# Optimization experiments

Measured on AMD Instinct MI355X. Metric: run time of the kernel, lower is better.

## Reference

```python
import jax, jax.numpy as jnp
import numpy as np

B, H, V, L, M, D, C = 64, 512, 50000, 400, 128, 64, 64
HC = 2 * D + M + 4  # controller LSTM hidden size (one head)
EPS = 1e-8


def _lstm_step(x, h, c, Wih, Whh, bih, bhh):
    g = x @ Wih.T + bih + h @ Whh.T + bhh
    i, f, gg, o = jnp.split(g, 4, axis=-1)
    c2 = jax.nn.sigmoid(f) * c + jax.nn.sigmoid(i) * jnp.tanh(gg)
    return jax.nn.sigmoid(o) * jnp.tanh(c2), c2


def _head_params(hc):
    # slices exactly as in LSTMMemoryController (k=0, single head)
    keys = hc[:, :M]                               # [B, M]
    kstr = jnp.exp(hc[:, D:D + 1])                 # [B, 1]
    gate = jax.nn.sigmoid(hc[:, D + 1:D + 2])      # [B, 1]
    erase = jax.nn.sigmoid(hc[:, D + 4:M + D + 4]) # [B, M]
    add = jax.nn.sigmoid(hc[:, 2 * D + 4:M + 2 * D + 4])  # [B, M]
    return keys, kstr, gate, erase, add


def _addressing(keys, kstr, gate, heads, memory):
    # torch cosine_similarity(keys.unsqueeze(2), memory, dim=2):
    # keys [B,M] broadcast along memory_dim D
    num = keys * memory.sum(-1)                                   # [B, M]
    nk = jnp.maximum(jnp.abs(keys) * jnp.sqrt(jnp.float32(D)), EPS)
    nm = jnp.maximum(jnp.linalg.norm(memory, axis=-1), EPS)
    cos = num / (nk * nm)
    content = jax.nn.softmax(kstr * cos, axis=1)                  # [B, M]
    # faithful to original: heads[k] indexes axis 0 (k=0) -> shape [1, M]
    gated = gate * content + (1.0 - gate) * heads[0]
    return gated[:, None, :]                                      # [B, 1, M]


def reference(input_ids, h0, c0, encoder_outputs, word_occurrence_indicator,
              coverage, memory, read_heads, write_heads,
              read_h, read_c, write_h, write_c,
              emb, attn_W, attn_b, cov_W, state_W, comb_W, comb_b,
              rpre_W, rpre_b, wpre_W, wpre_b,
              r_Wih, r_Whh, r_bih, r_bhh,
              w_Wih, w_Whh, w_bih, w_bhh,
              l_Wih, l_Whh, l_bih, l_bhh,
              out_W, out_b):
    embedded = emb[input_ids]                                     # [B, H]
    ia = jnp.concatenate([embedded, h0], 1) @ attn_W.T + attn_b  # [B, L]
    tc = (coverage + ia) @ cov_W.T
    ts = c0 @ state_W.T
    aw = jax.nn.softmax(tc + ia + ts, axis=1)                     # [B, L]
    attn_applied = jnp.einsum('bl,blh->bh', aw, encoder_outputs)  # [B, H]
    out0 = jnp.concatenate([embedded, attn_applied], 1) @ comb_W.T + comb_b  # [B, H]

    hm = jnp.concatenate([h0, memory.reshape(-1, M * D)], 1)
    rh, rc = _lstm_step(hm @ rpre_W.T + rpre_b, read_h, read_c, r_Wih, r_Whh, r_bih, r_bhh)
    wh, wc = _lstm_step(hm @ wpre_W.T + wpre_b, write_h, write_c, w_Wih, w_Whh, w_bih, w_bhh)
    rk, rks, rg, _, _ = _head_params(rh)
    wk, wks, wg, we, wa = _head_params(wh)
    rw = _addressing(rk, rks, rg, read_heads, memory)             # [B, 1, M]
    ww = _addressing(wk, wks, wg, write_heads, memory)            # [B, 1, M]

    read_in = jnp.einsum('bkm,bmd->bkd', rw, memory).reshape(-1, D)
    h1, c1 = _lstm_step(jnp.concatenate([out0, read_in], 1), h0, c0,
                        l_Wih, l_Whh, l_bih, l_bhh)
    # residual (h1 + out0) is computed in the original but unused by its output path

    w0 = ww[:, 0, :, None]                                        # [B, M, 1]
    new_memory = memory * (1.0 - w0 * we[:, :, None]) + w0 * wa[:, :, None]
    new_coverage = coverage + ia

    log_probs = jax.nn.log_softmax(c1[:, None, :] @ out_W.T + out_b, axis=-1)  # [B, 1, V]
    return log_probs, h1, c1, new_memory, new_coverage


def setup_inputs() -> dict:
    key = jax.random.key(0)
    ks = iter(jax.random.split(key, 48))

    def rn(shape, fan_in):
        return jax.random.normal(next(ks), shape, jnp.float32) / np.sqrt(fan_in)

    inp = {
        'input_ids': jax.random.randint(next(ks), (B,), 0, V),
        'h0': jax.random.normal(next(ks), (B, H), jnp.float32),
        'c0': jax.random.normal(next(ks), (B, H), jnp.float32),
        'encoder_outputs': jax.random.normal(next(ks), (B, L, H), jnp.float32),
        'word_occurrence_indicator': jnp.zeros((B, L), jnp.float32),
        'coverage': jnp.zeros((B, L), jnp.float32),
        'memory': jax.random.normal(next(ks), (B, M, D), jnp.float32),
        'read_heads': jnp.zeros((B, 1, M), jnp.float32),
        'write_heads': jnp.zeros((B, 1, M), jnp.float32),
        'read_h': jnp.zeros((B, HC), jnp.float32),
        'read_c': jnp.zeros((B, HC), jnp.float32),
        'write_h': jnp.zeros((B, HC), jnp.float32),
        'write_c': jnp.zeros((B, HC), jnp.float32),
        'emb': rn((V, H), H),
        'attn_W': rn((L, 2 * H), 2 * H), 'attn_b': jnp.zeros((L,), jnp.float32),
        'cov_W': rn((L, L), L),
        'state_W': rn((L, H), H),
        'comb_W': rn((H, 2 * H), 2 * H), 'comb_b': jnp.zeros((H,), jnp.float32),
        'rpre_W': rn((C, M * D + H), M * D + H), 'rpre_b': jnp.zeros((C,), jnp.float32),
        'wpre_W': rn((C, M * D + H), M * D + H), 'wpre_b': jnp.zeros((C,), jnp.float32),
        'r_Wih': rn((4 * HC, C), C), 'r_Whh': rn((4 * HC, HC), HC),
        'r_bih': jnp.zeros((4 * HC,), jnp.float32), 'r_bhh': jnp.zeros((4 * HC,), jnp.float32),
        'w_Wih': rn((4 * HC, C), C), 'w_Whh': rn((4 * HC, HC), HC),
        'w_bih': jnp.zeros((4 * HC,), jnp.float32), 'w_bhh': jnp.zeros((4 * HC,), jnp.float32),
        'l_Wih': rn((4 * H, H + D), H + D), 'l_Whh': rn((4 * H, H), H),
        'l_bih': jnp.zeros((4 * H,), jnp.float32), 'l_bhh': jnp.zeros((4 * H,), jnp.float32),
        'out_W': rn((V, H), H), 'out_b': jnp.zeros((V,), jnp.float32),
    }
    return inp
```

## Files before the change

### kernel.cpp

```cpp
#include <hip/hip_runtime.h>
#include <math.h>

#define BB 64
#define HH 512
#define VV 50000
#define LL 400
#define MM 128
#define DD 64
#define HC 260
#define EPSF 1e-8f

typedef __attribute__((ext_vector_type(8))) short bf16x8;
typedef __attribute__((ext_vector_type(4))) float f32x4;
typedef __attribute__((address_space(1))) const void CGV;
typedef __attribute__((address_space(3))) void LV;

__device__ __forceinline__ float sigmoidf(float x){ return 1.0f/(1.0f+expf(-x)); }
__device__ __forceinline__ unsigned short bf16_rne(float f){
  unsigned u = __float_as_uint(f);
  return (unsigned short)((u + 0x7fffu + ((u >> 16) & 1u)) >> 16);
}
__device__ __forceinline__ float wave_max(float v){
  #pragma unroll
  for(int o=32;o;o>>=1) v = fmaxf(v, __shfl_xor(v,o));
  return v;
}
__device__ __forceinline__ float wave_sum(float v){
  #pragma unroll
  for(int o=32;o;o>>=1) v += __shfl_xor(v,o);
  return v;
}

__global__ void k_embed(const int* __restrict__ ids, const float* __restrict__ emb,
                        const float* __restrict__ h0, float* __restrict__ xcat1,
                        float* __restrict__ xcat2){
  int idx = blockIdx.x*256 + threadIdx.x;
  if (idx >= BB*HH) return;
  int b = idx >> 9, h = idx & 511;
  float e = emb[(long)ids[b]*HH + h];
  xcat1[b*1024 + h] = e;
  xcat2[b*1024 + h] = e;
  xcat1[b*1024 + 512 + h] = h0[idx];
}

template<int NB, int FUSE>
__global__ __launch_bounds__(256) void k_gemv(const float* __restrict__ A,
                                              const float* __restrict__ A2,
                                              const float* __restrict__ W,
                                              const float* __restrict__ b1,
                                              float* __restrict__ C,
                                              int K, int N, int ldc){
  int b = blockIdx.y;
  int wid = threadIdx.x >> 6, lane = threadIdx.x & 63;
  int n = blockIdx.x*4 + wid;
  if (n >= N) return;
  const float4* A4  = (const float4*)(A + (long)b*K);
  const float4* A24 = (const float4*)(A2 + (long)b*K);
  const float4* W4  = (const float4*)(W + (long)n*K);
  int K4 = K >> 2;
  float acc = 0.f;
  for (int k = lane; k < K4; k += 64){
    float4 a = A4[k];
    if (FUSE){ float4 a2 = A24[k]; a.x+=a2.x; a.y+=a2.y; a.z+=a2.z; a.w+=a2.w; }
    float4 w = W4[k];
    acc += a.x*w.x + a.y*w.y + a.z*w.z + a.w*w.w;
  }
  acc = wave_sum(acc);
  if (lane == 0){
    if (NB) acc += b1[n];
    C[(long)b*ldc + n] = acc;
  }
}

__global__ void k_cov(const float* __restrict__ cov, const float* __restrict__ ia,
                      float* __restrict__ out){
  int idx = blockIdx.x*256 + threadIdx.x;
  if (idx >= BB*LL) return;
  out[idx] = cov[idx] + ia[idx];
}

__global__ __launch_bounds__(256) void k_softmax_aw(const float* __restrict__ ia,
                                                    const float* __restrict__ ts,
                                                    const float* __restrict__ tc,
                                                    float* __restrict__ aw){
  int b = blockIdx.x, t = threadIdx.x;
  int i0 = t, i1 = t + 256;
  float x0 = ia[b*LL+i0] + ts[b*LL+i0] + tc[b*LL+i0];
  float x1 = (i1 < LL) ? (ia[b*LL+i1] + ts[b*LL+i1] + tc[b*LL+i1]) : -INFINITY;
  __shared__ float sm[4], ss[4];
  float m = wave_max(fmaxf(x0, x1));
  if ((t & 63) == 0) sm[t>>6] = m;
  __syncthreads();
  m = fmaxf(fmaxf(sm[0], sm[1]), fmaxf(sm[2], sm[3]));
  float e0 = expf(x0 - m);
  float e1 = (i1 < LL) ? expf(x1 - m) : 0.0f;
  float s = wave_sum(e0 + e1);
  if ((t & 63) == 0) ss[t>>6] = s;
  __syncthreads();
  float tot = ss[0] + ss[1] + ss[2] + ss[3];
  float inv = 1.0f / tot;
  aw[b*LL + i0] = e0 * inv;
  if (i1 < LL) aw[b*LL + i1] = e1 * inv;
}

__global__ __launch_bounds__(256) void k_attn_part(const float* __restrict__ aw,
                                                   const float* __restrict__ enc,
                                                   float* __restrict__ part){
  int b = blockIdx.x, lc = blockIdx.y, t = threadIdx.x;
  const float* awb = aw + b*LL + lc*25;
  const float* eb  = enc + ((long)b*LL + lc*25)*HH;
  float a0 = 0.f, a1 = 0.f;
  for (int l = 0; l < 25; l++){
    float a = awb[l];
    a0 += a * eb[(long)l*HH + t];
    a1 += a * eb[(long)l*HH + t + 256];
  }
  part[((b*16 + lc) << 9) + t]       = a0;
  part[((b*16 + lc) << 9) + t + 256] = a1;
}

__global__ void k_attn_reduce(const float* __restrict__ part, float* __restrict__ xcat2){
  int idx = blockIdx.x*256 + threadIdx.x;
  if (idx >= BB*HH) return;
  int b = idx >> 9, h = idx & 511;
  float s = 0.f;
  #pragma unroll
  for (int lc = 0; lc < 16; lc++) s += part[((b*16 + lc) << 9) + h];
  xcat2[b*1024 + 512 + h] = s;
}

__global__ __launch_bounds__(256) void k_pre_gemv(const float* __restrict__ h0,
                                                  const float* __restrict__ mem,
                                                  const float* __restrict__ rW,
                                                  const float* __restrict__ wW,
                                                  float* __restrict__ part){
  int wid = threadIdx.x >> 6, lane = threadIdx.x & 63;
  int n = blockIdx.x*4 + wid;
  int b = blockIdx.y;
  int z = blockIdx.z;
  int which = z >> 3, chunk = z & 7;
  const float* W = which ? wW : rW;
  const float4* W4 = (const float4*)(W + (long)n*8704 + chunk*1088);
  const float4* H4 = (const float4*)(h0 + (long)b*HH);
  const float4* M4 = (const float4*)(mem + (long)b*8192 + (chunk*1088 - 512));
  float acc = 0.f;
  #pragma unroll
  for (int i = 0; i < 5; i++){
    int k4 = lane + i*64;
    if (k4 < 272){
      int kg4 = chunk*272 + k4;
      float4 a = (kg4 < 128) ? H4[kg4] : M4[k4];
      float4 w = W4[k4];
      acc += a.x*w.x + a.y*w.y + a.z*w.z + a.w*w.w;
    }
  }
  acc = wave_sum(acc);
  if (lane == 0) part[z*4096 + b*64 + n] = acc;
}

__global__ void k_pre_reduce(const float* __restrict__ part, const float* __restrict__ rb,
                             const float* __restrict__ wb, float* __restrict__ pre_r,
                             float* __restrict__ pre_w){
  int idx = blockIdx.x*256 + threadIdx.x;
  if (idx >= 8192) return;
  int which = idx >> 12;
  int r = idx & 4095;
  float s = 0.f;
  #pragma unroll
  for (int c = 0; c < 8; c++) s += part[((which<<3)+c)*4096 + r];
  int n = r & 63;
  s += which ? wb[n] : rb[n];
  (which ? pre_w : pre_r)[r] = s;
}

__global__ __launch_bounds__(256) void k_gates_rw(const float* __restrict__ pre_r,
    const float* __restrict__ pre_w, const float* __restrict__ read_h,
    const float* __restrict__ write_h,
    const float* __restrict__ rWih, const float* __restrict__ rWhh,
    const float* __restrict__ rbih, const float* __restrict__ rbhh,
    const float* __restrict__ wWih, const float* __restrict__ wWhh,
    const float* __restrict__ wbih, const float* __restrict__ wbhh,
    float* __restrict__ g_r, float* __restrict__ g_w){
  int which = blockIdx.z;
  int b = blockIdx.y;
  int wid = threadIdx.x >> 6, lane = threadIdx.x & 63;
  int n = blockIdx.x*4 + wid;
  const float* pre = which ? pre_w : pre_r;
  const float* hh  = which ? write_h : read_h;
  const float* Wih = which ? wWih : rWih;
  const float* Whh = which ? wWhh : rWhh;
  float acc = pre[b*64 + lane] * Wih[n*64 + lane];
  const float* hb = hh + b*HC;
  const float* wr = Whh + (long)n*HC;
  #pragma unroll
  for (int i = 0; i < 5; i++){
    int k = lane + i*64;
    if (k < HC) acc += hb[k]*wr[k];
  }
  acc = wave_sum(acc);
  if (lane == 0){
    acc += (which ? wbih : rbih)[n] + (which ? wbhh : rbhh)[n];
    (which ? g_w : g_r)[(long)b*4*HC + n] = acc;
  }
}

__global__ void k_lstm_rw(const float* __restrict__ g_r, const float* __restrict__ g_w,
                          const float* __restrict__ read_c, const float* __restrict__ write_c,
                          float* __restrict__ rh, float* __restrict__ wh){
  int idx = blockIdx.x*256 + threadIdx.x;
  if (idx >= 2*BB*HC) return;
  int which = idx >= BB*HC;
  int r = which ? idx - BB*HC : idx;
  int b = r / HC, j = r - b*HC;
  const float* g = (which ? g_w : g_r) + (long)b*4*HC;
  float c2 = sigmoidf(g[HC + j]) * (which ? write_c : read_c)[r]
           + sigmoidf(g[j]) * tanhf(g[2*HC + j]);
  (which ? wh : rh)[r] = sigmoidf(g[3*HC + j]) * tanhf(c2);
}

__global__ __launch_bounds__(128) void k_address(const float* __restrict__ rh,
                                                 const float* __restrict__ whv,
                                                 const float* __restrict__ rheads,
                                                 const float* __restrict__ wheads,
                                                 const float* __restrict__ mem,
                                                 float* __restrict__ rwout,
                                                 float* __restrict__ wwout){
  int which = blockIdx.y;
  int b = blockIdx.x, m = threadIdx.x;
  const float* hc = which ? whv : rh;
  const float* heads0 = which ? wheads : rheads;
  float* wout = which ? wwout : rwout;
  const float* mr = mem + ((long)b*MM + m)*DD;
  float s = 0.f, q = 0.f;
  #pragma unroll 8
  for (int d = 0; d < DD; d++){ float v = mr[d]; s += v; q += v*v; }
  float key  = hc[b*HC + m];
  float kstr = expf(hc[b*HC + 64]);
  float gate = sigmoidf(hc[b*HC + 65]);
  float nk = fmaxf(fabsf(key)*8.0f, EPSF);
  float nm = fmaxf(sqrtf(q), EPSF);
  float z  = kstr * (key*s) / (nk*nm);
  __shared__ float sm[2], ss[2];
  float mx = wave_max(z);
  if ((m & 63) == 0) sm[m>>6] = mx;
  __syncthreads();
  mx = fmaxf(sm[0], sm[1]);
  float e = expf(z - mx);
  float w = wave_sum(e);
  if ((m & 63) == 0) ss[m>>6] = w;
  __syncthreads();
  float content = e / (ss[0] + ss[1]);
  wout[b*MM + m] = gate*content + (1.0f - gate)*heads0[m];
}

__global__ void k_readin(const float* __restrict__ rw, const float* __restrict__ mem,
                         float* __restrict__ xcat3){
  int b = blockIdx.x, d = threadIdx.x;
  float s = 0.f;
  for (int m = 0; m < MM; m++) s += rw[b*MM + m] * mem[((long)b*MM + m)*DD + d];
  xcat3[b*576 + 512 + d] = s;
}

__global__ void k_newmem(const float* __restrict__ mem, const float* __restrict__ ww,
                         const float* __restrict__ wh, float* __restrict__ out){
  int idx = blockIdx.x*256 + threadIdx.x;
  if (idx >= BB*MM*DD) return;
  int b = idx >> 13;
  int m = (idx & 8191) >> 6;
  float w0 = ww[b*MM + m];
  float we = sigmoidf(wh[b*HC + 68 + m]);
  float wa = sigmoidf(wh[b*HC + 132 + m]);
  out[idx] = mem[idx]*(1.0f - w0*we) + w0*wa;
}

__global__ __launch_bounds__(256) void k_lstm_main(const float* __restrict__ xcat3,
                                                   const float* __restrict__ h0,
                                                   const float* __restrict__ lWih,
                                                   const float* __restrict__ lWhh,
                                                   const float* __restrict__ bih,
                                                   const float* __restrict__ bhh,
                                                   const float* __restrict__ c0,
                                                   float* __restrict__ h1,
                                                   float* __restrict__ c1,
                                                   unsigned short* __restrict__ c1b){
  int wid = threadIdx.x >> 6, lane = threadIdx.x & 63;
  int j = blockIdx.x*4 + wid;
  int b = blockIdx.y;
  const float4* A1 = (const float4*)(xcat3 + (long)b*576);
  const float4* A2 = (const float4*)(h0 + (long)b*HH);
  float gv[4];
  #pragma unroll
  for (int g = 0; g < 4; g++){
    int n = g*HH + j;
    const float4* W1 = (const float4*)(lWih + (long)n*576);
    const float4* W2 = (const float4*)(lWhh + (long)n*HH);
    float s = 0.f;
    #pragma unroll
    for (int i = 0; i < 3; i++){
      int k = lane + i*64;
      if (k < 144){ float4 a = A1[k], w = W1[k]; s += a.x*w.x + a.y*w.y + a.z*w.z + a.w*w.w; }
    }
    #pragma unroll
    for (int i = 0; i < 2; i++){
      int k = lane + i*64;
      float4 a = A2[k], w = W2[k]; s += a.x*w.x + a.y*w.y + a.z*w.z + a.w*w.w;
    }
    gv[g] = wave_sum(s);
  }
  if (lane == 0){
    #pragma unroll
    for (int g = 0; g < 4; g++){ int n = g*HH + j; gv[g] += bih[n] + bhh[n]; }
    float c2 = sigmoidf(gv[1])*c0[b*HH + j] + sigmoidf(gv[0])*tanhf(gv[2]);
    h1[b*HH + j] = sigmoidf(gv[3])*tanhf(c2);
    c1[b*HH + j] = c2;
    c1b[b*HH + j] = bf16_rne(c2);
  }
}

__global__ __launch_bounds__(128) void k_logits_mfma(const unsigned short* __restrict__ Ab,
                                                     const float* __restrict__ W,
                                                     const float* __restrict__ bias,
                                                     float* __restrict__ C){
  __shared__ float lds[16384];
  int wid = threadIdx.x >> 6, lane = threadIdx.x & 63;
  int strip = blockIdx.x*2 + wid;
  if (strip >= 3125) return;
  int nl = lane & 15;
  int q  = lane >> 4;
  int n  = strip*16 + nl;
  const float* Wlane = W + (long)n*HH + q*4;
  int base = wid*8192;

  #pragma unroll
  for (int ci = 0; ci < 32; ci++)
    __builtin_amdgcn_global_load_lds((CGV*)(Wlane + ci*16),
        (LV*)&lds[base + ci*256], 16, 0, 0);
  asm volatile("s_waitcnt vmcnt(0)" ::: "memory");
  __builtin_amdgcn_sched_barrier(0);

  const bf16x8* A0 = (const bf16x8*)Ab + (long)(0*16 + nl)*64 + q;
  const bf16x8* A1 = (const bf16x8*)Ab + (long)(1*16 + nl)*64 + q;
  const bf16x8* A2 = (const bf16x8*)Ab + (long)(2*16 + nl)*64 + q;
  const bf16x8* A3 = (const bf16x8*)Ab + (long)(3*16 + nl)*64 + q;
  f32x4 acc0 = {0.f,0.f,0.f,0.f}, acc1 = acc0, acc2 = acc0, acc3 = acc0;

  #pragma unroll
  for (int ks = 0; ks < 16; ks++){
    int off = base + (ks*2 + (q>>1))*256 + (q&1)*128 + nl*4;
    float4 w0 = *(const float4*)&lds[off];
    float4 w1 = *(const float4*)&lds[off + 64];
    bf16x8 bf;
    bf[0] = (short)bf16_rne(w0.x); bf[1] = (short)bf16_rne(w0.y);
    bf[2] = (short)bf16_rne(w0.z); bf[3] = (short)bf16_rne(w0.w);
    bf[4] = (short)bf16_rne(w1.x); bf[5] = (short)bf16_rne(w1.y);
    bf[6] = (short)bf16_rne(w1.z); bf[7] = (short)bf16_rne(w1.w);
    bf16x8 a0 = A0[ks*4];
    bf16x8 a1 = A1[ks*4];
    bf16x8 a2 = A2[ks*4];
    bf16x8 a3 = A3[ks*4];
    acc0 = __builtin_amdgcn_mfma_f32_16x16x32_bf16(a0, bf, acc0, 0, 0, 0);
    acc1 = __builtin_amdgcn_mfma_f32_16x16x32_bf16(a1, bf, acc1, 0, 0, 0);
    acc2 = __builtin_amdgcn_mfma_f32_16x16x32_bf16(a2, bf, acc2, 0, 0, 0);
    acc3 = __builtin_amdgcn_mfma_f32_16x16x32_bf16(a3, bf, acc3, 0, 0, 0);
  }
  float bv = bias[n];
  #pragma unroll
  for (int r = 0; r < 4; r++){
    int m = q*4 + r;
    C[(long)(m     )*VV + n] = acc0[r] + bv;
    C[(long)(m + 16)*VV + n] = acc1[r] + bv;
    C[(long)(m + 32)*VV + n] = acc2[r] + bv;
    C[(long)(m + 48)*VV + n] = acc3[r] + bv;
  }
}

__global__ __launch_bounds__(256) void k_ls1(const float* __restrict__ lp,
                                             float* __restrict__ pm, float* __restrict__ ps){
  int b = blockIdx.y, c = blockIdx.x, t = threadIdx.x;
  const float* row = lp + (long)b*VV + c*2000;
  float mx = -INFINITY;
  for (int i = t; i < 2000; i += 256) mx = fmaxf(mx, row[i]);
  __shared__ float sm[4], ss[4];
  mx = wave_max(mx);
  if ((t & 63) == 0) sm[t>>6] = mx;
  __syncthreads();
  mx = fmaxf(fmaxf(sm[0], sm[1]), fmaxf(sm[2], sm[3]));
  float s = 0.f;
  for (int i = t; i < 2000; i += 256) s += expf(row[i] - mx);
  s = wave_sum(s);
  if ((t & 63) == 0) ss[t>>6] = s;
  __syncthreads();
  if (t == 0){ pm[b*25 + c] = mx; ps[b*25 + c] = ss[0]+ss[1]+ss[2]+ss[3]; }
}

__global__ void k_ls2(const float* __restrict__ pm, const float* __restrict__ ps,
                      float* __restrict__ lse){
  int b = threadIdx.x;
  float m = -INFINITY;
  for (int c = 0; c < 25; c++) m = fmaxf(m, pm[b*25 + c]);
  float s = 0.f;
  for (int c = 0; c < 25; c++) s += ps[b*25 + c]*expf(pm[b*25 + c] - m);
  lse[b] = m + logf(s);
}

__global__ void k_ls3(float* __restrict__ lp, const float* __restrict__ lse){
  int idx = blockIdx.x*256 + threadIdx.x;
  if (idx >= BB*VV) return;
  int b = idx / VV;
  lp[idx] -= lse[b];
}

extern "C" void kernel_launch(void* const* d_in, const int* in_sizes, int n_in,
                              void* d_out, int out_size, void* d_ws, size_t ws_size,
                              hipStream_t stream) {
  const int*   ids     = (const int*)  d_in[0];
  const float* h0      = (const float*)d_in[1];
  const float* c0      = (const float*)d_in[2];
  const float* enc     = (const float*)d_in[3];
  const float* cov     = (const float*)d_in[5];
  const float* mem     = (const float*)d_in[6];
  const float* rheads  = (const float*)d_in[7];
  const float* wheads  = (const float*)d_in[8];
  const float* read_h  = (const float*)d_in[9];
  const float* read_c  = (const float*)d_in[10];
  const float* write_h = (const float*)d_in[11];
  const float* write_c = (const float*)d_in[12];
  const float* emb     = (const float*)d_in[13];
  const float* attn_W  = (const float*)d_in[14];
  const float* attn_b  = (const float*)d_in[15];
  const float* cov_W   = (const float*)d_in[16];
  const float* state_W = (const float*)d_in[17];
  const float* comb_W  = (const float*)d_in[18];
  const float* comb_b  = (const float*)d_in[19];
  const float* rpre_W  = (const float*)d_in[20];
  const float* rpre_b  = (const float*)d_in[21];
  const float* wpre_W  = (const float*)d_in[22];
  const float* wpre_b  = (const float*)d_in[23];
  const float* r_Wih   = (const float*)d_in[24];
  const float* r_Whh   = (const float*)d_in[25];
  const float* r_bih   = (const float*)d_in[26];
  const float* r_bhh   = (const float*)d_in[27];
  const float* w_Wih   = (const float*)d_in[28];
  const float* w_Whh   = (const float*)d_in[29];
  const float* w_bih   = (const float*)d_in[30];
  const float* w_bhh   = (const float*)d_in[31];
  const float* l_Wih   = (const float*)d_in[32];
  const float* l_Whh   = (const float*)d_in[33];
  const float* l_bih   = (const float*)d_in[34];
  const float* l_bhh   = (const float*)d_in[35];
  const float* out_W   = (const float*)d_in[36];
  const float* out_b   = (const float*)d_in[37];

  float* out  = (float*)d_out;
  float* lp   = out;
  float* h1   = out + 3200000;
  float* c1   = h1 + 32768;
  float* nmem = c1 + 32768;
  float* ncov = nmem + 524288;

  float* w = (float*)d_ws;
  float* xcat1 = w;
  float* xcat2 = xcat1 + 65536;
  float* xcat3 = xcat2 + 65536;
  float* ia    = xcat3 + 36864;
  float* ts    = ia + 25600;
  float* tc    = ts + 25600;
  float* aw    = tc + 25600;
  float* U     = aw + 25600;
  float* pre_r = U + 557056;
  float* pre_w = pre_r + 4096;
  float* g_r   = pre_w + 4096;
  float* g_w   = g_r + 66560;
  float* rh    = g_w + 66560;
  float* wh    = rh + 16640;
  float* rw    = wh + 16640;
  float* wwgt  = rw + 8192;
  float* pm    = wwgt + 8192;
  float* ps    = pm + 1600;
  float* lse   = ps + 1600;
  unsigned short* c1b = (unsigned short*)(lse + 64);

  k_embed<<<128, 256, 0, stream>>>(ids, emb, h0, xcat1, xcat2);
  k_gemv<1,0><<<dim3(100,64), 256, 0, stream>>>(xcat1, xcat1, attn_W, attn_b, ia, 1024, LL, LL);
  k_gemv<0,0><<<dim3(100,64), 256, 0, stream>>>(c0, c0, state_W, nullptr, ts, HH, LL, LL);
  k_cov<<<100, 256, 0, stream>>>(cov, ia, ncov);
  k_gemv<0,1><<<dim3(100,64), 256, 0, stream>>>(cov, ia, cov_W, nullptr, tc, LL, LL, LL);
  k_softmax_aw<<<64, 256, 0, stream>>>(ia, ts, tc, aw);
  k_attn_part<<<dim3(64,16), 256, 0, stream>>>(aw, enc, U);
  k_attn_reduce<<<128, 256, 0, stream>>>(U, xcat2);
  k_gemv<1,0><<<dim3(128,64), 256, 0, stream>>>(xcat2, xcat2, comb_W, comb_b, xcat3, 1024, HH, 576);

  k_pre_gemv<<<dim3(16,64,16), 256, 0, stream>>>(h0, mem, rpre_W, wpre_W, U);
  k_pre_reduce<<<32, 256, 0, stream>>>(U, rpre_b, wpre_b, pre_r, pre_w);

  k_gates_rw<<<dim3(260,64,2), 256, 0, stream>>>(pre_r, pre_w, read_h, write_h,
      r_Wih, r_Whh, r_bih, r_bhh, w_Wih, w_Whh, w_bih, w_bhh, g_r, g_w);
  k_lstm_rw<<<130, 256, 0, stream>>>(g_r, g_w, read_c, write_c, rh, wh);

  k_address<<<dim3(64,2), 128, 0, stream>>>(rh, wh, rheads, wheads, mem, rw, wwgt);
  k_readin<<<64, 64, 0, stream>>>(rw, mem, xcat3);
  k_newmem<<<2048, 256, 0, stream>>>(mem, wwgt, wh, nmem);

  k_lstm_main<<<dim3(128,64), 256, 0, stream>>>(xcat3, h0, l_Wih, l_Whh, l_bih, l_bhh,
                                                c0, h1, c1, c1b);

  k_logits_mfma<<<1563, 128, 0, stream>>>(c1b, out_W, out_b, lp);
  k_ls1<<<dim3(25,64), 256, 0, stream>>>(lp, pm, ps);
  k_ls2<<<1, 64, 0, stream>>>(pm, ps, lse);
  k_ls3<<<12500, 256, 0, stream>>>(lp, lse);
}
```

Before: 511.2 us.

## Fuse front-end kernels to cut launches and intermediate buffers

Merges the embedding gather into the attention and combine GEMVs, runs the ia and ts GEMVs in a single launch, and folds the coverage update into the tc GEMV. The softmax moves into the attention partial-sum kernel, the controller gate GEMVs are fused with their LSTM cell update, and addressing is fused with the memory read and the new-memory write. The pre-projection GEMV loses its split-K chunking and reduce kernel. Launch count and global round-trips drop from about 17 to 8 small kernels, but the un-split pre GEMV has far fewer blocks and the new-memory write now runs on only 64 blocks, which may reduce parallelism.

New measurement: 479.1 us. 1.07x faster.

```diff
diff --git a/kernel.cpp b/kernel.cpp
--- a/kernel.cpp
+++ b/kernel.cpp
@@ -30,88 +30,98 @@
   for(int o=32;o;o>>=1) v += __shfl_xor(v,o);
   return v;
 }
-
-__global__ void k_embed(const int* __restrict__ ids, const float* __restrict__ emb,
-                        const float* __restrict__ h0, float* __restrict__ xcat1,
-                        float* __restrict__ xcat2){
-  int idx = blockIdx.x*256 + threadIdx.x;
-  if (idx >= BB*HH) return;
-  int b = idx >> 9, h = idx & 511;
-  float e = emb[(long)ids[b]*HH + h];
-  xcat1[b*1024 + h] = e;
-  xcat2[b*1024 + h] = e;
-  xcat1[b*1024 + 512 + h] = h0[idx];
-}
-
-template<int NB, int FUSE>
-__global__ __launch_bounds__(256) void k_gemv(const float* __restrict__ A,
-                                              const float* __restrict__ A2,
-                                              const float* __restrict__ W,
-                                              const float* __restrict__ b1,
-                                              float* __restrict__ C,
-                                              int K, int N, int ldc){
+__device__ __forceinline__ float dot4(float4 a, float4 w){
+  return a.x*w.x + a.y*w.y + a.z*w.z + a.w*w.w;
+}
+
+__global__ __launch_bounds__(256) void k_ia_ts(const int* __restrict__ ids,
+    const float* __restrict__ emb, const float* __restrict__ h0,
+    const float* __restrict__ c0, const float* __restrict__ attn_W,
+    const float* __restrict__ attn_b, const float* __restrict__ state_W,
+    float* __restrict__ ia, float* __restrict__ ts){
   int b = blockIdx.y;
   int wid = threadIdx.x >> 6, lane = threadIdx.x & 63;
+  if (blockIdx.x < 100){
+    int n = blockIdx.x*4 + wid;
+    const float4* E4 = (const float4*)(emb + (long)ids[b]*HH);
+    const float4* H4 = (const float4*)(h0 + (long)b*HH);
+    const float4* W4 = (const float4*)(attn_W + (long)n*1024);
+    float acc = 0.f;
+    #pragma unroll
+    for (int i = 0; i < 4; i++){
+      int k = lane + i*64;
+      float4 a = (k < 128) ? E4[k] : H4[k-128];
+      acc += dot4(a, W4[k]);
+    }
+    acc = wave_sum(acc);
+    if (lane == 0) ia[b*LL + n] = acc + attn_b[n];
+  } else {
+    int n = (blockIdx.x-100)*4 + wid;
+    const float4* A4 = (const float4*)(c0 + (long)b*HH);
+    const float4* W4 = (const float4*)(state_W + (long)n*HH);
+    float acc = 0.f;
+    #pragma unroll
+    for (int i = 0; i < 2; i++){
+      int k = lane + i*64;
+      acc += dot4(A4[k], W4[k]);
+    }
+    acc = wave_sum(acc);
+    if (lane == 0) ts[b*LL + n] = acc;
+  }
+}
+
+__global__ __launch_bounds__(256) void k_tc_cov(const float* __restrict__ cov,
+    const float* __restrict__ ia, const float* __restrict__ cov_W,
+    float* __restrict__ tc, float* __restrict__ ncov){
+  int b = blockIdx.y;
+  int wid = threadIdx.x >> 6, lane = threadIdx.x & 63;
   int n = blockIdx.x*4 + wid;
-  if (n >= N) return;
-  const float4* A4  = (const float4*)(A + (long)b*K);
-  const float4* A24 = (const float4*)(A2 + (long)b*K);
-  const float4* W4  = (const float4*)(W + (long)n*K);
-  int K4 = K >> 2;
+  const float4* C4 = (const float4*)(cov + (long)b*LL);
+  const float4* I4 = (const float4*)(ia + (long)b*LL);
+  const float4* W4 = (const float4*)(cov_W + (long)n*LL);
   float acc = 0.f;
-  for (int k = lane; k < K4; k += 64){
-    float4 a = A4[k];
-    if (FUSE){ float4 a2 = A24[k]; a.x+=a2.x; a.y+=a2.y; a.z+=a2.z; a.w+=a2.w; }
-    float4 w = W4[k];
-    acc += a.x*w.x + a.y*w.y + a.z*w.z + a.w*w.w;
+  #pragma unroll
+  for (int i = 0; i < 2; i++){
+    int k = lane + i*64;
+    if (k < 100){
+      float4 a = C4[k], a2 = I4[k], w = W4[k];
+      acc += (a.x+a2.x)*w.x + (a.y+a2.y)*w.y + (a.z+a2.z)*w.z + (a.w+a2.w)*w.w;
+    }
   }
   acc = wave_sum(acc);
   if (lane == 0){
-    if (NB) acc += b1[n];
-    C[(long)b*ldc + n] = acc;
-  }
-}
-
-__global__ void k_cov(const float* __restrict__ cov, const float* __restrict__ ia,
-                      float* __restrict__ out){
-  int idx = blockIdx.x*256 + threadIdx.x;
-  if (idx >= BB*LL) return;
-  out[idx] = cov[idx] + ia[idx];
-}
-
-__global__ __launch_bounds__(256) void k_softmax_aw(const float* __restrict__ ia,
-                                                    const float* __restrict__ ts,
-                                                    const float* __restrict__ tc,
-                                                    float* __restrict__ aw){
-  int b = blockIdx.x, t = threadIdx.x;
+    tc[b*LL + n] = acc;
+    ncov[b*LL + n] = cov[b*LL + n] + ia[b*LL + n];
+  }
+}
+
+__global__ __launch_bounds__(256) void k_attn_part(const float* __restrict__ ia,
+                                                   const float* __restrict__ ts,
+                                                   const float* __restrict__ tc,
+                                                   const float* __restrict__ enc,
+                                                   float* __restrict__ part){
+  int b = blockIdx.x, lc = blockIdx.y, t = threadIdx.x;
+  __shared__ float sh[400];
+  __shared__ float sm[4], ss[4];
   int i0 = t, i1 = t + 256;
   float x0 = ia[b*LL+i0] + ts[b*LL+i0] + tc[b*LL+i0];
   float x1 = (i1 < LL) ? (ia[b*LL+i1] + ts[b*LL+i1] + tc[b*LL+i1]) : -INFINITY;
-  __shared__ float sm[4], ss[4];
   float m = wave_max(fmaxf(x0, x1));
   if ((t & 63) == 0) sm[t>>6] = m;
   __syncthreads();
   m = fmaxf(fmaxf(sm[0], sm[1]), fmaxf(sm[2], sm[3]));
   float e0 = expf(x0 - m);
   float e1 = (i1 < LL) ? expf(x1 - m) : 0.0f;
+  sh[i0] = e0;
+  if (i1 < LL) sh[i1] = e1;
   float s = wave_sum(e0 + e1);
   if ((t & 63) == 0) ss[t>>6] = s;
   __syncthreads();
-  float tot = ss[0] + ss[1] + ss[2] + ss[3];
-  float inv = 1.0f / tot;
-  aw[b*LL + i0] = e0 * inv;
-  if (i1 < LL) aw[b*LL + i1] = e1 * inv;
-}
-
-__global__ __launch_bounds__(256) void k_attn_part(const float* __restrict__ aw,
-                                                   const float* __restrict__ enc,
-                                                   float* __restrict__ part){
-  int b = blockIdx.x, lc = blockIdx.y, t = threadIdx.x;
-  const float* awb = aw + b*LL + lc*25;
-  const float* eb  = enc + ((long)b*LL + lc*25)*HH;
+  float inv = 1.0f / (ss[0] + ss[1] + ss[2] + ss[3]);
+  const float* eb = enc + ((long)b*LL + lc*25)*HH;
   float a0 = 0.f, a1 = 0.f;
   for (int l = 0; l < 25; l++){
-    float a = awb[l];
+    float a = sh[lc*25 + l] * inv;
     a0 += a * eb[(long)l*HH + t];
     a1 += a * eb[(long)l*HH + t + 256];
   }
@@ -119,117 +129,112 @@
   part[((b*16 + lc) << 9) + t + 256] = a1;
 }
 
-__global__ void k_attn_reduce(const float* __restrict__ part, float* __restrict__ xcat2){
+__global__ void k_attn_reduce(const float* __restrict__ part, float* __restrict__ attn){
   int idx = blockIdx.x*256 + threadIdx.x;
   if (idx >= BB*HH) return;
   int b = idx >> 9, h = idx & 511;
   float s = 0.f;
   #pragma unroll
   for (int lc = 0; lc < 16; lc++) s += part[((b*16 + lc) << 9) + h];
-  xcat2[b*1024 + 512 + h] = s;
-}
-
-__global__ __launch_bounds__(256) void k_pre_gemv(const float* __restrict__ h0,
-                                                  const float* __restrict__ mem,
-                                                  const float* __restrict__ rW,
-                                                  const float* __restrict__ wW,
-                                                  float* __restrict__ part){
+  attn[b*HH + h] = s;
+}
+
+__global__ __launch_bounds__(256) void k_comb(const int* __restrict__ ids,
+    const float* __restrict__ emb, const float* __restrict__ attn,
+    const float* __restrict__ comb_W, const float* __restrict__ comb_b,
+    float* __restrict__ xcat3){
+  int b = blockIdx.y;
+  int wid = threadIdx.x >> 6, lane = threadIdx.x & 63;
+  int n = blockIdx.x*4 + wid;
+  const float4* E4 = (const float4*)(emb + (long)ids[b]*HH);
+  const float4* A4 = (const float4*)(attn + (long)b*HH);
+  const float4* W4 = (const float4*)(comb_W + (long)n*1024);
+  float acc = 0.f;
+  #pragma unroll
+  for (int i = 0; i < 4; i++){
+    int k = lane + i*64;
+    float4 a = (k < 128) ? E4[k] : A4[k-128];
+    acc += dot4(a, W4[k]);
+  }
+  acc = wave_sum(acc);
+  if (lane == 0) xcat3[b*576 + n] = acc + comb_b[n];
+}
+
+__global__ __launch_bounds__(256) void k_pre(const float* __restrict__ h0,
+    const float* __restrict__ mem, const float* __restrict__ rW,
+    const float* __restrict__ wW, const float* __restrict__ rb,
+    const float* __restrict__ wb, float* __restrict__ pre_r,
+    float* __restrict__ pre_w){
   int wid = threadIdx.x >> 6, lane = threadIdx.x & 63;
   int n = blockIdx.x*4 + wid;
   int b = blockIdx.y;
-  int z = blockIdx.z;
-  int which = z >> 3, chunk = z & 7;
+  int which = blockIdx.z;
   const float* W = which ? wW : rW;
-  const float4* W4 = (const float4*)(W + (long)n*8704 + chunk*1088);
+  const float4* W4 = (const float4*)(W + (long)n*8704);
   const float4* H4 = (const float4*)(h0 + (long)b*HH);
-  const float4* M4 = (const float4*)(mem + (long)b*8192 + (chunk*1088 - 512));
+  const float4* M4 = (const float4*)(mem + (long)b*8192);
   float acc = 0.f;
-  #pragma unroll
-  for (int i = 0; i < 5; i++){
-    int k4 = lane + i*64;
-    if (k4 < 272){
-      int kg4 = chunk*272 + k4;
-      float4 a = (kg4 < 128) ? H4[kg4] : M4[k4];
-      float4 w = W4[k4];
-      acc += a.x*w.x + a.y*w.y + a.z*w.z + a.w*w.w;
-    }
+  #pragma unroll 4
+  for (int i = 0; i < 34; i++){
+    int k = lane + i*64;
+    float4 a = (k < 128) ? H4[k] : M4[k-128];
+    acc += dot4(a, W4[k]);
   }
   acc = wave_sum(acc);
-  if (lane == 0) part[z*4096 + b*64 + n] = acc;
-}
-
-__global__ void k_pre_reduce(const float* __restrict__ part, const float* __restrict__ rb,
-                             const float* __restrict__ wb, float* __restrict__ pre_r,
-                             float* __restrict__ pre_w){
-  int idx = blockIdx.x*256 + threadIdx.x;
-  if (idx >= 8192) return;
-  int which = idx >> 12;
-  int r = idx & 4095;
-  float s = 0.f;
-  #pragma unroll
-  for (int c = 0; c < 8; c++) s += part[((which<<3)+c)*4096 + r];
-  int n = r & 63;
-  s += which ? wb[n] : rb[n];
-  (which ? pre_w : pre_r)[r] = s;
-}
-
-__global__ __launch_bounds__(256) void k_gates_rw(const float* __restrict__ pre_r,
+  if (lane == 0) (which ? pre_w : pre_r)[b*64 + n] = acc + (which ? wb : rb)[n];
+}
+
+__global__ __launch_bounds__(256) void k_gates(const float* __restrict__ pre_r,
     const float* __restrict__ pre_w, const float* __restrict__ read_h,
-    const float* __restrict__ write_h,
+    const float* __restrict__ write_h, const float* __restrict__ read_c,
+    const float* __restrict__ write_c,
     const float* __restrict__ rWih, const float* __restrict__ rWhh,
     const float* __restrict__ rbih, const float* __restrict__ rbhh,
     const float* __restrict__ wWih, const float* __restrict__ wWhh,
     const float* __restrict__ wbih, const float* __restrict__ wbhh,
-    float* __restrict__ g_r, float* __restrict__ g_w){
-  int which = blockIdx.z;
-  int b = blockIdx.y;
-  int wid = threadIdx.x >> 6, lane = threadIdx.x & 63;
-  int n = blockIdx.x*4 + wid;
+    float* __restrict__ rh, float* __restrict__ wh){
+  int which = blockIdx.z, b = blockIdx.y;
+  int wid = threadIdx.x >> 6, lane = threadIdx.x & 63;
+  int j = blockIdx.x*4 + wid;
   const float* pre = which ? pre_w : pre_r;
-  const float* hh  = which ? write_h : read_h;
+  const float* hhv = which ? write_h : read_h;
   const float* Wih = which ? wWih : rWih;
   const float* Whh = which ? wWhh : rWhh;
-  float acc = pre[b*64 + lane] * Wih[n*64 + lane];
-  const float* hb = hh + b*HC;
-  const float* wr = Whh + (long)n*HC;
-  #pragma unroll
-  for (int i = 0; i < 5; i++){
-    int k = lane + i*64;
-    if (k < HC) acc += hb[k]*wr[k];
-  }
-  acc = wave_sum(acc);
+  float pv = pre[b*64 + lane];
+  const float* hb = hhv + b*HC;
+  float gv[4];
+  #pragma unroll
+  for (int g = 0; g < 4; g++){
+    int n = g*HC + j;
+    float acc = pv * Wih[n*64 + lane];
+    const float* wr = Whh + (long)n*HC;
+    #pragma unroll
+    for (int i = 0; i < 5; i++){
+      int k = lane + i*64;
+      if (k < HC) acc += hb[k]*wr[k];
+    }
+    gv[g] = wave_sum(acc);
+  }
   if (lane == 0){
-    acc += (which ? wbih : rbih)[n] + (which ? wbhh : rbhh)[n];
-    (which ? g_w : g_r)[(long)b*4*HC + n] = acc;
-  }
-}
-
-__global__ void k_lstm_rw(const float* __restrict__ g_r, const float* __restrict__ g_w,
-                          const float* __restrict__ read_c, const float* __restrict__ write_c,
-                          float* __restrict__ rh, float* __restrict__ wh){
-  int idx = blockIdx.x*256 + threadIdx.x;
-  if (idx >= 2*BB*HC) return;
-  int which = idx >= BB*HC;
-  int r = which ? idx - BB*HC : idx;
-  int b = r / HC, j = r - b*HC;
-  const float* g = (which ? g_w : g_r) + (long)b*4*HC;
-  float c2 = sigmoidf(g[HC + j]) * (which ? write_c : read_c)[r]
-           + sigmoidf(g[j]) * tanhf(g[2*HC + j]);
-  (which ? wh : rh)[r] = sigmoidf(g[3*HC + j]) * tanhf(c2);
-}
-
-__global__ __launch_bounds__(128) void k_address(const float* __restrict__ rh,
-                                                 const float* __restrict__ whv,
-                                                 const float* __restrict__ rheads,
-                                                 const float* __restrict__ wheads,
-                                                 const float* __restrict__ mem,
-                                                 float* __restrict__ rwout,
-                                                 float* __restrict__ wwout){
+    #pragma unroll
+    for (int g = 0; g < 4; g++) gv[g] += (which ? wbih : rbih)[g*HC+j] + (which ? wbhh : rbhh)[g*HC+j];
+    float c2 = sigmoidf(gv[1]) * (which ? write_c : read_c)[b*HC + j]
+             + sigmoidf(gv[0]) * tanhf(gv[2]);
+    (which ? wh : rh)[b*HC + j] = sigmoidf(gv[3]) * tanhf(c2);
+  }
+}
+
+__global__ __launch_bounds__(128) void k_addr_mem(const float* __restrict__ rh,
+                                                  const float* __restrict__ whv,
+                                                  const float* __restrict__ rheads,
+                                                  const float* __restrict__ wheads,
+                                                  const float* __restrict__ mem,
+                                                  float* __restrict__ xcat3,
+                                                  float* __restrict__ nmem){
   int which = blockIdx.y;
   int b = blockIdx.x, m = threadIdx.x;
   const float* hc = which ? whv : rh;
   const float* heads0 = which ? wheads : rheads;
-  float* wout = which ? wwout : rwout;
   const float* mr = mem + ((long)b*MM + m)*DD;
   float s = 0.f, q = 0.f;
   #pragma unroll 8
@@ -241,6 +246,7 @@
   float nm = fmaxf(sqrtf(q), EPSF);
   float z  = kstr * (key*s) / (nk*nm);
   __shared__ float sm[2], ss[2];
+  __shared__ float wsh[128], weL[128], waL[128];
   float mx = wave_max(z);
   if ((m & 63) == 0) sm[m>>6] = mx;
   __syncthreads();
@@ -250,27 +256,26 @@
   if ((m & 63) == 0) ss[m>>6] = w;
   __syncthreads();
   float content = e / (ss[0] + ss[1]);
-  wout[b*MM + m] = gate*content + (1.0f - gate)*heads0[m];
-}
-
-__global__ void k_readin(const float* __restrict__ rw, const float* __restrict__ mem,
-                         float* __restrict__ xcat3){
-  int b = blockIdx.x, d = threadIdx.x;
-  float s = 0.f;
-  for (int m = 0; m < MM; m++) s += rw[b*MM + m] * mem[((long)b*MM + m)*DD + d];
-  xcat3[b*576 + 512 + d] = s;
-}
-
-__global__ void k_newmem(const float* __restrict__ mem, const float* __restrict__ ww,
-                         const float* __restrict__ wh, float* __restrict__ out){
-  int idx = blockIdx.x*256 + threadIdx.x;
-  if (idx >= BB*MM*DD) return;
-  int b = idx >> 13;
-  int m = (idx & 8191) >> 6;
-  float w0 = ww[b*MM + m];
-  float we = sigmoidf(wh[b*HC + 68 + m]);
-  float wa = sigmoidf(wh[b*HC + 132 + m]);
-  out[idx] = mem[idx]*(1.0f - w0*we) + w0*wa;
+  float wv = gate*content + (1.0f - gate)*heads0[m];
+  wsh[m] = wv;
+  if (which){
+    weL[m] = sigmoidf(whv[b*HC + 68 + m]);
+    waL[m] = sigmoidf(whv[b*HC + 132 + m]);
+  }
+  __syncthreads();
+  if (!which){
+    if (m < DD){
+      float acc = 0.f;
+      #pragma unroll 8
+      for (int mm = 0; mm < MM; mm++) acc += wsh[mm] * mem[((long)b*MM + mm)*DD + m];
+      xcat3[b*576 + 512 + m] = acc;
+    }
+  } else {
+    for (int idx = m; idx < MM*DD; idx += 128){
+      int mm = idx >> 6;
+      nmem[(long)b*8192 + idx] = mem[(long)b*8192 + idx]*(1.0f - wsh[mm]*weL[mm]) + wsh[mm]*waL[mm];
+    }
+  }
 }
 
 __global__ __launch_bounds__(256) void k_lstm_main(const float* __restrict__ xcat3,
@@ -298,12 +303,12 @@
     #pragma unroll
     for (int i = 0; i < 3; i++){
       int k = lane + i*64;
-      if (k < 144){ float4 a = A1[k], w = W1[k]; s += a.x*w.x + a.y*w.y + a.z*w.z + a.w*w.w; }
+      if (k < 144){ s += dot4(A1[k], W1[k]); }
     }
     #pragma unroll
     for (int i = 0; i < 2; i++){
       int k = lane + i*64;
-      float4 a = A2[k], w = W2[k]; s += a.x*w.x + a.y*w.y + a.z*w.z + a.w*w.w;
+      s += dot4(A2[k], W2[k]);
     }
     gv[g] = wave_sum(s);
   }
@@ -459,47 +464,31 @@
   float* ncov = nmem + 524288;
 
   float* w = (float*)d_ws;
-  float* xcat1 = w;
-  float* xcat2 = xcat1 + 65536;
-  float* xcat3 = xcat2 + 65536;
+  float* xcat3 = w;
   float* ia    = xcat3 + 36864;
   float* ts    = ia + 25600;
   float* tc    = ts + 25600;
-  float* aw    = tc + 25600;
-  float* U     = aw + 25600;
-  float* pre_r = U + 557056;
+  float* attn  = tc + 25600;
+  float* U     = attn + 32768;
+  float* pre_r = U + 524288;
   float* pre_w = pre_r + 4096;
-  float* g_r   = pre_w + 4096;
-  float* g_w   = g_r + 66560;
-  float* rh    = g_w + 66560;
+  float* rh    = pre_w + 4096;
   float* wh    = rh + 16640;
-  float* rw    = wh + 16640;
-  float* wwgt  = rw + 8192;
-  float* pm    = wwgt + 8192;
+  float* pm    = wh + 16640;
   float* ps    = pm + 1600;
   float* lse   = ps + 1600;
   unsigned short* c1b = (unsigned short*)(lse + 64);
 
-  k_embed<<<128, 256, 0, stream>>>(ids, emb, h0, xcat1, xcat2);
-  k_gemv<1,0><<<dim3(100,64), 256, 0, stream>>>(xcat1, xcat1, attn_W, attn_b, ia, 1024, LL, LL);
-  k_gemv<0,0><<<dim3(100,64), 256, 0, stream>>>(c0, c0, state_W, nullptr, ts, HH, LL, LL);
-  k_cov<<<100, 256, 0, stream>>>(cov, ia, ncov);
-  k_gemv<0,1><<<dim3(100,64), 256, 0, stream>>>(cov, ia, cov_W, nullptr, tc, LL, LL, LL);
-  k_softmax_aw<<<64, 256, 0, stream>>>(ia, ts, tc, aw);
-  k_attn_part<<<dim3(64,16), 256, 0, stream>>>(aw, enc, U);
-  k_attn_reduce<<<128, 256, 0, stream>>>(U, xcat2);
-  k_gemv<1,0><<<dim3(128,64), 256, 0, stream>>>(xcat2, xcat2, comb_W, comb_b, xcat3, 1024, HH, 576);
-
-  k_pre_gemv<<<dim3(16,64,16), 256, 0, stream>>>(h0, mem, rpre_W, wpre_W, U);
-  k_pre_reduce<<<32, 256, 0, stream>>>(U, rpre_b, wpre_b, pre_r, pre_w);
-
-  k_gates_rw<<<dim3(260,64,2), 256, 0, stream>>>(pre_r, pre_w, read_h, write_h,
-      r_Wih, r_Whh, r_bih, r_bhh, w_Wih, w_Whh, w_bih, w_bhh, g_r, g_w);
-  k_lstm_rw<<<130, 256, 0, stream>>>(g_r, g_w, read_c, write_c, rh, wh);
-
-  k_address<<<dim3(64,2), 128, 0, stream>>>(rh, wh, rheads, wheads, mem, rw, wwgt);
-  k_readin<<<64, 64, 0, stream>>>(rw, mem, xcat3);
-  k_newmem<<<2048, 256, 0, stream>>>(mem, wwgt, wh, nmem);
+  k_ia_ts<<<dim3(200,64), 256, 0, stream>>>(ids, emb, h0, c0, attn_W, attn_b, state_W, ia, ts);
+  k_tc_cov<<<dim3(100,64), 256, 0, stream>>>(cov, ia, cov_W, tc, ncov);
+  k_attn_part<<<dim3(64,16), 256, 0, stream>>>(ia, ts, tc, enc, U);
+  k_attn_reduce<<<128, 256, 0, stream>>>(U, attn);
+  k_comb<<<dim3(128,64), 256, 0, stream>>>(ids, emb, attn, comb_W, comb_b, xcat3);
+
+  k_pre<<<dim3(16,64,2), 256, 0, stream>>>(h0, mem, rpre_W, wpre_W, rpre_b, wpre_b, pre_r, pre_w);
+  k_gates<<<dim3(65,64,2), 256, 0, stream>>>(pre_r, pre_w, read_h, write_h, read_c, write_c,
+      r_Wih, r_Whh, r_bih, r_bhh, w_Wih, w_Whh, w_bih, w_bhh, rh, wh);
+  k_addr_mem<<<dim3(64,2), 128, 0, stream>>>(rh, wh, rheads, wheads, mem, xcat3, nmem);
 
   k_lstm_main<<<dim3(128,64), 256, 0, stream>>>(xcat3, h0, l_Wih, l_Whh, l_bih, l_bhh,
                                                 c0, h1, c1, c1b);
```
